# Optimization experiments

Measured on AMD Instinct MI355X. Metric: run time of the kernel, lower is better.

## Reference

```python
import jax, jax.numpy as jnp
import numpy as np

B, T, C, H = 4, 2048, 768, 64

def setup_inputs() -> dict:
    key = jax.random.key(0)
    k1, k2, k3, k4 = jax.random.split(key, 4)
    x = jax.random.normal(k1, (B, T, C), dtype=jnp.float32)
    # Dense kernels (glorot-ish scale)
    s = 1.0 / np.sqrt(C)
    Wq = jax.random.normal(k2, (C, H), dtype=jnp.float32) * s
    Wk = jax.random.normal(k3, (C, H), dtype=jnp.float32) * s
    Wv = jax.random.normal(k4, (C, H), dtype=jnp.float32) * s
    return {"x": x, "Wq": Wq, "Wk": Wk, "Wv": Wv}

def reference(x, Wq, Wk, Wv):
    # q, k, v: [B, T, H]
    q = jnp.einsum('btc,ch->bth', x, Wq)
    k = jnp.einsum('btc,ch->bth', x, Wk)
    v = jnp.einsum('btc,ch->bth', x, Wv)
    scale = k.shape[-1] ** -0.5
    # scores: [B, T, T]
    scores = jnp.einsum('bth,bsh->bts', q, k) * scale
    # causal mask: lower-triangular allowed
    causal = jnp.tril(jnp.ones((T, T), dtype=bool))
    scores = jnp.where(causal, scores, -jnp.inf)
    weights = jax.nn.softmax(scores, axis=-1)
    # dropout is inactive at inference (Keras default training=False)
    out = jnp.einsum('bts,bsh->bth', weights, v)
    return out
```

## Files before the change

### kernel.cpp

```cpp
#include <hip/hip_runtime.h>
#include <hip/hip_bf16.h>
#include <math.h>

constexpr int BB = 4;
constexpr int TT = 2048;
constexpr int CC = 768;
constexpr int HH = 64;
constexpr int NSPLIT = 8;

#define QSCALE 0.1803368801111204f

typedef __attribute__((ext_vector_type(8))) short bf16x8;
typedef __attribute__((ext_vector_type(4))) float f32x4;

__device__ inline ushort f2bf(float f) {
    uint u = __float_as_uint(f);
    u += 0x7fffu + ((u >> 16) & 1u);
    return (ushort)(u >> 16);
}

__device__ inline float fexp2(float x) { return __builtin_amdgcn_exp2f(x); }

__device__ inline bf16x8 cvt8(const float4 a, const float4 b) {
    union { bf16x8 v; __hip_bfloat162 h[4]; } u;
    u.h[0] = __float22bfloat162_rn(make_float2(a.x, a.y));
    u.h[1] = __float22bfloat162_rn(make_float2(a.z, a.w));
    u.h[2] = __float22bfloat162_rn(make_float2(b.x, b.y));
    u.h[3] = __float22bfloat162_rn(make_float2(b.z, b.w));
    return u.v;
}

__global__ __launch_bounds__(256) void prep_w(const float* __restrict__ Wq,
                                              const float* __restrict__ Wk,
                                              const float* __restrict__ Wv,
                                              ushort* __restrict__ Wt) {
    const int k0  = blockIdx.x * 64;
    const int mat = blockIdx.y;
    const float* W = (mat == 0) ? Wq : (mat == 1) ? Wk : Wv;
    __shared__ ushort tile[64 * 66];
    const int tid = threadIdx.x;

    for (int i = tid; i < 1024; i += 256) {
        int kk = i >> 4, c = i & 15;
        float4 f = ((const float4*)W)[(k0 + kk) * 16 + c];
        ushort* d = &tile[kk * 66 + c * 4];
        d[0] = f2bf(f.x); d[1] = f2bf(f.y); d[2] = f2bf(f.z); d[3] = f2bf(f.w);
    }
    __syncthreads();
    for (int i = tid; i < 512; i += 256) {
        int n = i >> 3, c8 = i & 7;
        bf16x8 v;
        #pragma unroll
        for (int j = 0; j < 8; ++j)
            ((ushort*)&v)[j] = tile[(c8 * 8 + j) * 66 + n];
        *(bf16x8*)&Wt[(size_t)(mat * 64 + n) * CC + k0 + c8 * 8] = v;
    }
}

__global__ __launch_bounds__(256) void qkv_mfma(const float* __restrict__ x,
                                                const ushort* __restrict__ Wt,
                                                ushort* __restrict__ qg,
                                                ushort* __restrict__ kg,
                                                ushort* __restrict__ vtg) {
    __shared__ ushort vts[64 * 24];
    const int tid  = threadIdx.x;
    const int row0 = blockIdx.x * 16;
    const int lane = tid & 63, w = tid >> 6;
    const int l15  = lane & 15, quad = lane >> 4;
    const int cg   = w * 48;

    f32x4 acc[3];
    #pragma unroll
    for (int i = 0; i < 3; ++i) acc[i] = (f32x4){0.f, 0.f, 0.f, 0.f};

    const float*  xrow  = x + (size_t)(row0 + l15) * CC;
    const ushort* wbase = Wt + (size_t)(cg + l15) * CC + quad * 8;

    float4 xb[4][2];
    bf16x8 wb[4][3];
    #pragma unroll
    for (int i = 0; i < 4; ++i) {
        const float4* xp = (const float4*)(xrow + i * 32) + quad * 2;
        xb[i][0] = xp[0];
        xb[i][1] = xp[1];
        #pragma unroll
        for (int nt = 0; nt < 3; ++nt)
            wb[i][nt] = *(const bf16x8*)(wbase + (size_t)nt * 16 * CC + i * 32);
    }

    #pragma unroll
    for (int kc = 0; kc < 24; ++kc) {
        const int cur = kc & 3;
        bf16x8 a  = cvt8(xb[cur][0], xb[cur][1]);
        bf16x8 w0 = wb[cur][0], w1 = wb[cur][1], w2 = wb[cur][2];
        const int nx = kc + 4;
        if (nx < 24) {
            const float4* xp = (const float4*)(xrow + nx * 32) + quad * 2;
            xb[cur][0] = xp[0];
            xb[cur][1] = xp[1];
            #pragma unroll
            for (int nt = 0; nt < 3; ++nt)
                wb[cur][nt] = *(const bf16x8*)(wbase + (size_t)nt * 16 * CC + nx * 32);
        }
        acc[0] = __builtin_amdgcn_mfma_f32_16x16x32_bf16(a, w0, acc[0], 0, 0, 0);
        acc[1] = __builtin_amdgcn_mfma_f32_16x16x32_bf16(a, w1, acc[1], 0, 0, 0);
        acc[2] = __builtin_amdgcn_mfma_f32_16x16x32_bf16(a, w2, acc[2], 0, 0, 0);
    }

    #pragma unroll
    for (int nt = 0; nt < 3; ++nt) {
        int n = cg + nt * 16 + l15;
        #pragma unroll
        for (int r = 0; r < 4; ++r) {
            int row = row0 + quad * 4 + r;
            float vacc = acc[nt][r];
            if (n < 64)       qg[(size_t)row * HH + n] = f2bf(vacc * QSCALE);
            else if (n < 128) kg[(size_t)row * HH + (n - 64)] = f2bf(vacc);
            else              vts[(n - 128) * 24 + (quad * 4 + r)] = f2bf(vacc);
        }
    }
    __syncthreads();
    if (tid < 128) {
        int h = tid >> 1, p = tid & 1;
        int b = row0 >> 11, tl = row0 & 2047;
        bf16x8 v = *(const bf16x8*)&vts[h * 24 + p * 8];
        *(bf16x8*)&vtg[(size_t)b * (HH * TT) + (size_t)h * TT + tl + p * 8] = v;
    }
}

__global__ __launch_bounds__(128) void attn_split(const ushort* __restrict__ qg,
                                                  const ushort* __restrict__ kg,
                                                  const ushort* __restrict__ vtg,
                                                  float* __restrict__ Op,
                                                  float* __restrict__ ml) {
    const int qt2 = blockIdx.x, b = blockIdx.y, split = blockIdx.z;
    const int tid  = threadIdx.x;
    const int lane = tid & 63, w = tid >> 6;
    const int l15  = lane & 15, quad = lane >> 4;
    const int t0   = qt2 * 32;
    const int pidx = ((b * 64 + qt2) << 3) + split;

    const int ntile = (qt2 >> 1) + 1;
    const int lo = (ntile * split) >> 3;
    const int hi = (ntile * (split + 1)) >> 3;

    if (lo >= hi) {
        float4 z = (float4){0.f, 0.f, 0.f, 0.f};
        float4* op4 = (float4*)(Op + (size_t)pidx * 2048);
        #pragma unroll
        for (int j = 0; j < 4; ++j) op4[tid * 4 + j] = z;
        if (tid < 32) {
            ml[pidx * 64 + tid]      = -1e30f;
            ml[pidx * 64 + 32 + tid] = 0.f;
        }
        return;
    }

    __shared__ ushort Ps[2][16 * 72];

    const ushort* qp = &qg[(size_t)(b * TT + t0 + w * 16 + l15) * HH + quad * 8];
    bf16x8 qa0 = *(const bf16x8*)qp;
    bf16x8 qa1 = *(const bf16x8*)(qp + 32);

    const ushort* kbb = &kg[(size_t)(b * TT + l15) * HH + quad * 8];
    const ushort* vbb = &vtg[(size_t)b * (HH * TT) + (size_t)l15 * TT + quad * 8];

    f32x4 po[4];
    #pragma unroll
    for (int i = 0; i < 4; ++i) po[i] = (f32x4){0.f, 0.f, 0.f, 0.f};
    float mrun[4] = {-1e30f, -1e30f, -1e30f, -1e30f};
    float lrun[4] = {0.f, 0.f, 0.f, 0.f};

    bf16x8 kb[8], vb[8];
    #pragma unroll
    for (int nt = 0; nt < 4; ++nt) {
        const ushort* kp = kbb + (size_t)(lo * 64 + nt * 16) * HH;
        kb[2 * nt]     = *(const bf16x8*)kp;
        kb[2 * nt + 1] = *(const bf16x8*)(kp + 32);
    }

    for (int st = lo; st < hi; ++st) {
        f32x4 sf[4];
        #pragma unroll
        for (int nt = 0; nt < 4; ++nt) {
            f32x4 z = (f32x4){0.f, 0.f, 0.f, 0.f};
            z = __builtin_amdgcn_mfma_f32_16x16x32_bf16(qa0, kb[2 * nt], z, 0, 0, 0);
            sf[nt] = __builtin_amdgcn_mfma_f32_16x16x32_bf16(qa1, kb[2 * nt + 1], z, 0, 0, 0);
        }
        if (st + 1 < hi) {
            #pragma unroll
            for (int nt = 0; nt < 4; ++nt) {
                const ushort* kp = kbb + (size_t)((st + 1) * 64 + nt * 16) * HH;
                kb[2 * nt]     = *(const bf16x8*)kp;
                kb[2 * nt + 1] = *(const bf16x8*)(kp + 32);
            }
        }
        #pragma unroll
        for (int jj = 0; jj < 4; ++jj) {
            const ushort* vp = vbb + (size_t)(jj * 16) * TT + st * 64;
            vb[2 * jj]     = *(const bf16x8*)vp;
            vb[2 * jj + 1] = *(const bf16x8*)(vp + 32);
        }

        float p[4][4];
        float rm[4] = {-1e30f, -1e30f, -1e30f, -1e30f};
        if (st == ntile - 1) {
            #pragma unroll
            for (int nt = 0; nt < 4; ++nt) {
                int s_abs = st * 64 + nt * 16 + l15;
                #pragma unroll
                for (int r = 0; r < 4; ++r) {
                    int t_abs = t0 + w * 16 + quad * 4 + r;
                    float v = (s_abs > t_abs) ? -1e30f : sf[nt][r];
                    p[nt][r] = v;
                    rm[r] = fmaxf(rm[r], v);
                }
            }
        } else {
            #pragma unroll
            for (int nt = 0; nt < 4; ++nt)
                #pragma unroll
                for (int r = 0; r < 4; ++r) {
                    p[nt][r] = sf[nt][r];
                    rm[r] = fmaxf(rm[r], sf[nt][r]);
                }
        }
        float alpha[4], rs[4] = {0.f, 0.f, 0.f, 0.f};
        #pragma unroll
        for (int r = 0; r < 4; ++r) {
            float v = rm[r];
            v = fmaxf(v, __shfl_xor(v, 1, 64));
            v = fmaxf(v, __shfl_xor(v, 2, 64));
            v = fmaxf(v, __shfl_xor(v, 4, 64));
            v = fmaxf(v, __shfl_xor(v, 8, 64));
            float mnew = fmaxf(mrun[r], v);
            alpha[r] = fexp2(mrun[r] - mnew);
            mrun[r] = mnew;
        }
        #pragma unroll
        for (int nt = 0; nt < 4; ++nt)
            #pragma unroll
            for (int r = 0; r < 4; ++r) {
                float e = fexp2(p[nt][r] - mrun[r]);
                p[nt][r] = e;
                rs[r] += e;
            }
        #pragma unroll
        for (int r = 0; r < 4; ++r) {
            float v = rs[r];
            v += __shfl_xor(v, 1, 64);
            v += __shfl_xor(v, 2, 64);
            v += __shfl_xor(v, 4, 64);
            v += __shfl_xor(v, 8, 64);
            lrun[r] = lrun[r] * alpha[r] + v;
        }
        #pragma unroll
        for (int jj = 0; jj < 4; ++jj)
            #pragma unroll
            for (int r = 0; r < 4; ++r)
                po[jj][r] *= alpha[r];

        #pragma unroll
        for (int nt = 0; nt < 4; ++nt)
            #pragma unroll
            for (int r = 0; r < 4; ++r)
                Ps[w][(quad * 4 + r) * 72 + nt * 16 + l15] = f2bf(p[nt][r]);
        bf16x8 pa0 = *(const bf16x8*)&Ps[w][l15 * 72 + quad * 8];
        bf16x8 pa1 = *(const bf16x8*)&Ps[w][l15 * 72 + 32 + quad * 8];

        #pragma unroll
        for (int jj = 0; jj < 4; ++jj) {
            po[jj] = __builtin_amdgcn_mfma_f32_16x16x32_bf16(pa0, vb[2 * jj], po[jj], 0, 0, 0);
            po[jj] = __builtin_amdgcn_mfma_f32_16x16x32_bf16(pa1, vb[2 * jj + 1], po[jj], 0, 0, 0);
        }
    }

    #pragma unroll
    for (int jj = 0; jj < 4; ++jj)
        #pragma unroll
        for (int r = 0; r < 4; ++r)
            Op[(size_t)pidx * 2048 + (w * 16 + quad * 4 + r) * 64 + jj * 16 + l15] =
                po[jj][r];
    if (l15 == 0) {
        #pragma unroll
        for (int r = 0; r < 4; ++r) {
            int row = w * 16 + quad * 4 + r;
            ml[pidx * 64 + row]      = mrun[r];
            ml[pidx * 64 + 32 + row] = lrun[r];
        }
    }
}

__global__ __launch_bounds__(256) void attn_merge(const float* __restrict__ Op,
                                                  const float* __restrict__ ml,
                                                  float* __restrict__ out) {
    const int tid = threadIdx.x;
    const int w = tid >> 6, lane = tid & 63;
    const int row = blockIdx.x * 4 + w;
    const int b = row >> 11, t = row & 2047;
    const int qt2 = t >> 5, rl = t & 31;
    const int pbase = ((b * 64 + qt2) << 3);

    float m[NSPLIT], l[NSPLIT];
    #pragma unroll
    for (int i = 0; i < NSPLIT; ++i) {
        m[i] = ml[(pbase + i) * 64 + rl];
        l[i] = ml[(pbase + i) * 64 + 32 + rl];
    }
    float M = -1e30f;
    #pragma unroll
    for (int i = 0; i < NSPLIT; ++i) M = fmaxf(M, m[i]);
    float wgt[NSPLIT], L = 0.f;
    #pragma unroll
    for (int i = 0; i < NSPLIT; ++i) {
        wgt[i] = fexp2(m[i] - M);
        L += wgt[i] * l[i];
    }
    float acc = 0.f;
    #pragma unroll
    for (int i = 0; i < NSPLIT; ++i)
        acc += wgt[i] * Op[(size_t)(pbase + i) * 2048 + rl * 64 + lane];
    out[(size_t)row * HH + lane] = acc / L;
}

extern "C" void kernel_launch(void* const* d_in, const int* in_sizes, int n_in,
                              void* d_out, int out_size, void* d_ws, size_t ws_size,
                              hipStream_t stream)
{
    const float* x  = (const float*)d_in[0];
    const float* Wq = (const float*)d_in[1];
    const float* Wk = (const float*)d_in[2];
    const float* Wv = (const float*)d_in[3];
    float* out = (float*)d_out;

    ushort* qg  = (ushort*)d_ws;
    ushort* kg  = qg  + (size_t)BB * TT * HH;
    ushort* vtg = kg  + (size_t)BB * TT * HH;
    ushort* Wt  = vtg + (size_t)BB * TT * HH;
    float*  Op  = (float*)(Wt + (size_t)3 * HH * CC);
    float*  ml  = Op + (size_t)2048 * 2048;

    prep_w    <<<dim3(12, 3),           dim3(256), 0, stream>>>(Wq, Wk, Wv, Wt);
    qkv_mfma  <<<dim3((BB * TT) / 16),  dim3(256), 0, stream>>>(x, Wt, qg, kg, vtg);
    attn_split<<<dim3(64, BB, NSPLIT),  dim3(128), 0, stream>>>(qg, kg, vtg, Op, ml);
    attn_merge<<<dim3((BB * TT) / 4),   dim3(256), 0, stream>>>(Op, ml, out);
}
```

Baseline: 135.2 us.

## Fuse split-KV merge into attention kernel via last-block atomic counter

Removes the separate attn_merge launch. Each split block publishes its partial output and m/l statistics, fences, and increments a per-group atomic counter. The last-arriving block of each query group merges all eight partials and writes the final output. This saves a kernel launch and lets the merge read partials that are likely still in cache, at the cost of an added memset, atomics, fences and a serial merge done by a single 128-thread block per group.

```diff
diff --git a/kernel.cpp b/kernel.cpp
--- a/kernel.cpp
+++ b/kernel.cpp
@@ -128,21 +128,27 @@
     }
 }
 
-__global__ __launch_bounds__(128) void attn_split(const ushort* __restrict__ qg,
+__global__ __launch_bounds__(128) void attn_fused(const ushort* __restrict__ qg,
                                                   const ushort* __restrict__ kg,
                                                   const ushort* __restrict__ vtg,
                                                   float* __restrict__ Op,
-                                                  float* __restrict__ ml) {
+                                                  float* __restrict__ ml,
+                                                  int* __restrict__ cnt,
+                                                  float* __restrict__ out) {
     const int qt2 = blockIdx.x, b = blockIdx.y, split = blockIdx.z;
     const int tid  = threadIdx.x;
     const int lane = tid & 63, w = tid >> 6;
     const int l15  = lane & 15, quad = lane >> 4;
     const int t0   = qt2 * 32;
-    const int pidx = ((b * 64 + qt2) << 3) + split;
+    const int grp  = b * 64 + qt2;
+    const int pidx = (grp << 3) + split;
 
     const int ntile = (qt2 >> 1) + 1;
     const int lo = (ntile * split) >> 3;
     const int hi = (ntile * (split + 1)) >> 3;
+
+    __shared__ ushort Ps[2][16 * 72];
+    __shared__ int sOld;
 
     if (lo >= hi) {
         float4 z = (float4){0.f, 0.f, 0.f, 0.f};
@@ -153,174 +159,169 @@
             ml[pidx * 64 + tid]      = -1e30f;
             ml[pidx * 64 + 32 + tid] = 0.f;
         }
-        return;
-    }
-
-    __shared__ ushort Ps[2][16 * 72];
-
-    const ushort* qp = &qg[(size_t)(b * TT + t0 + w * 16 + l15) * HH + quad * 8];
-    bf16x8 qa0 = *(const bf16x8*)qp;
-    bf16x8 qa1 = *(const bf16x8*)(qp + 32);
-
-    const ushort* kbb = &kg[(size_t)(b * TT + l15) * HH + quad * 8];
-    const ushort* vbb = &vtg[(size_t)b * (HH * TT) + (size_t)l15 * TT + quad * 8];
-
-    f32x4 po[4];
-    #pragma unroll
-    for (int i = 0; i < 4; ++i) po[i] = (f32x4){0.f, 0.f, 0.f, 0.f};
-    float mrun[4] = {-1e30f, -1e30f, -1e30f, -1e30f};
-    float lrun[4] = {0.f, 0.f, 0.f, 0.f};
-
-    bf16x8 kb[8], vb[8];
-    #pragma unroll
-    for (int nt = 0; nt < 4; ++nt) {
-        const ushort* kp = kbb + (size_t)(lo * 64 + nt * 16) * HH;
-        kb[2 * nt]     = *(const bf16x8*)kp;
-        kb[2 * nt + 1] = *(const bf16x8*)(kp + 32);
-    }
-
-    for (int st = lo; st < hi; ++st) {
-        f32x4 sf[4];
+    } else {
+        const ushort* qp = &qg[(size_t)(b * TT + t0 + w * 16 + l15) * HH + quad * 8];
+        bf16x8 qa0 = *(const bf16x8*)qp;
+        bf16x8 qa1 = *(const bf16x8*)(qp + 32);
+
+        const ushort* kbb = &kg[(size_t)(b * TT + l15) * HH + quad * 8];
+        const ushort* vbb = &vtg[(size_t)b * (HH * TT) + (size_t)l15 * TT + quad * 8];
+
+        f32x4 po[4];
+        #pragma unroll
+        for (int i = 0; i < 4; ++i) po[i] = (f32x4){0.f, 0.f, 0.f, 0.f};
+        float mrun[4] = {-1e30f, -1e30f, -1e30f, -1e30f};
+        float lrun[4] = {0.f, 0.f, 0.f, 0.f};
+
+        bf16x8 kb[8], vb[8];
         #pragma unroll
         for (int nt = 0; nt < 4; ++nt) {
-            f32x4 z = (f32x4){0.f, 0.f, 0.f, 0.f};
-            z = __builtin_amdgcn_mfma_f32_16x16x32_bf16(qa0, kb[2 * nt], z, 0, 0, 0);
-            sf[nt] = __builtin_amdgcn_mfma_f32_16x16x32_bf16(qa1, kb[2 * nt + 1], z, 0, 0, 0);
-        }
-        if (st + 1 < hi) {
+            const ushort* kp = kbb + (size_t)(lo * 64 + nt * 16) * HH;
+            kb[2 * nt]     = *(const bf16x8*)kp;
+            kb[2 * nt + 1] = *(const bf16x8*)(kp + 32);
+        }
+
+        for (int st = lo; st < hi; ++st) {
+            f32x4 sf[4];
             #pragma unroll
             for (int nt = 0; nt < 4; ++nt) {
-                const ushort* kp = kbb + (size_t)((st + 1) * 64 + nt * 16) * HH;
-                kb[2 * nt]     = *(const bf16x8*)kp;
-                kb[2 * nt + 1] = *(const bf16x8*)(kp + 32);
-            }
-        }
-        #pragma unroll
-        for (int jj = 0; jj < 4; ++jj) {
-            const ushort* vp = vbb + (size_t)(jj * 16) * TT + st * 64;
-            vb[2 * jj]     = *(const bf16x8*)vp;
-            vb[2 * jj + 1] = *(const bf16x8*)(vp + 32);
-        }
-
-        float p[4][4];
-        float rm[4] = {-1e30f, -1e30f, -1e30f, -1e30f};
-        if (st == ntile - 1) {
-            #pragma unroll
-            for (int nt = 0; nt < 4; ++nt) {
-                int s_abs = st * 64 + nt * 16 + l15;
+                f32x4 z = (f32x4){0.f, 0.f, 0.f, 0.f};
+                z = __builtin_amdgcn_mfma_f32_16x16x32_bf16(qa0, kb[2 * nt], z, 0, 0, 0);
+                sf[nt] = __builtin_amdgcn_mfma_f32_16x16x32_bf16(qa1, kb[2 * nt + 1], z, 0, 0, 0);
+            }
+            if (st + 1 < hi) {
+                #pragma unroll
+                for (int nt = 0; nt < 4; ++nt) {
+                    const ushort* kp = kbb + (size_t)((st + 1) * 64 + nt * 16) * HH;
+                    kb[2 * nt]     = *(const bf16x8*)kp;
+                    kb[2 * nt + 1] = *(const bf16x8*)(kp + 32);
+                }
+            }
+            #pragma unroll
+            for (int jj = 0; jj < 4; ++jj) {
+                const ushort* vp = vbb + (size_t)(jj * 16) * TT + st * 64;
+                vb[2 * jj]     = *(const bf16x8*)vp;
+                vb[2 * jj + 1] = *(const bf16x8*)(vp + 32);
+            }
+
+            float p[4][4];
+            float rm[4] = {-1e30f, -1e30f, -1e30f, -1e30f};
+            if (st == ntile - 1) {
+                #pragma unroll
+                for (int nt = 0; nt < 4; ++nt) {
+                    int s_abs = st * 64 + nt * 16 + l15;
+                    #pragma unroll
+                    for (int r = 0; r < 4; ++r) {
+                        int t_abs = t0 + w * 16 + quad * 4 + r;
+                        float v = (s_abs > t_abs) ? -1e30f : sf[nt][r];
+                        p[nt][r] = v;
+                        rm[r] = fmaxf(rm[r], v);
+                    }
+                }
+            } else {
+                #pragma unroll
+                for (int nt = 0; nt < 4; ++nt)
+                    #pragma unroll
+                    for (int r = 0; r < 4; ++r) {
+                        p[nt][r] = sf[nt][r];
+                        rm[r] = fmaxf(rm[r], sf[nt][r]);
+                    }
+            }
+            float alpha[4], rs[4] = {0.f, 0.f, 0.f, 0.f};
+            #pragma unroll
+            for (int r = 0; r < 4; ++r) {
+                float v = rm[r];
+                v = fmaxf(v, __shfl_xor(v, 1, 64));
+                v = fmaxf(v, __shfl_xor(v, 2, 64));
+                v = fmaxf(v, __shfl_xor(v, 4, 64));
+                v = fmaxf(v, __shfl_xor(v, 8, 64));
+                float mnew = fmaxf(mrun[r], v);
+                alpha[r] = fexp2(mrun[r] - mnew);
+                mrun[r] = mnew;
+            }
+            #pragma unroll
+            for (int nt = 0; nt < 4; ++nt)
                 #pragma unroll
                 for (int r = 0; r < 4; ++r) {
-                    int t_abs = t0 + w * 16 + quad * 4 + r;
-                    float v = (s_abs > t_abs) ? -1e30f : sf[nt][r];
-                    p[nt][r] = v;
-                    rm[r] = fmaxf(rm[r], v);
+                    float e = fexp2(p[nt][r] - mrun[r]);
+                    p[nt][r] = e;
+                    rs[r] += e;
                 }
-            }
-        } else {
+            #pragma unroll
+            for (int r = 0; r < 4; ++r) {
+                float v = rs[r];
+                v += __shfl_xor(v, 1, 64);
+                v += __shfl_xor(v, 2, 64);
+                v += __shfl_xor(v, 4, 64);
+                v += __shfl_xor(v, 8, 64);
+                lrun[r] = lrun[r] * alpha[r] + v;
+            }
+            #pragma unroll
+            for (int jj = 0; jj < 4; ++jj)
+                #pragma unroll
+                for (int r = 0; r < 4; ++r)
+                    po[jj][r] *= alpha[r];
+
             #pragma unroll
             for (int nt = 0; nt < 4; ++nt)
                 #pragma unroll
-                for (int r = 0; r < 4; ++r) {
-                    p[nt][r] = sf[nt][r];
-                    rm[r] = fmaxf(rm[r], sf[nt][r]);
-                }
-        }
-        float alpha[4], rs[4] = {0.f, 0.f, 0.f, 0.f};
-        #pragma unroll
-        for (int r = 0; r < 4; ++r) {
-            float v = rm[r];
-            v = fmaxf(v, __shfl_xor(v, 1, 64));
-            v = fmaxf(v, __shfl_xor(v, 2, 64));
-            v = fmaxf(v, __shfl_xor(v, 4, 64));
-            v = fmaxf(v, __shfl_xor(v, 8, 64));
-            float mnew = fmaxf(mrun[r], v);
-            alpha[r] = fexp2(mrun[r] - mnew);
-            mrun[r] = mnew;
-        }
-        #pragma unroll
-        for (int nt = 0; nt < 4; ++nt)
+                for (int r = 0; r < 4; ++r)
+                    Ps[w][(quad * 4 + r) * 72 + nt * 16 + l15] = f2bf(p[nt][r]);
+            bf16x8 pa0 = *(const bf16x8*)&Ps[w][l15 * 72 + quad * 8];
+            bf16x8 pa1 = *(const bf16x8*)&Ps[w][l15 * 72 + 32 + quad * 8];
+
+            #pragma unroll
+            for (int jj = 0; jj < 4; ++jj) {
+                po[jj] = __builtin_amdgcn_mfma_f32_16x16x32_bf16(pa0, vb[2 * jj], po[jj], 0, 0, 0);
+                po[jj] = __builtin_amdgcn_mfma_f32_16x16x32_bf16(pa1, vb[2 * jj + 1], po[jj], 0, 0, 0);
+            }
+        }
+
+        #pragma unroll
+        for (int jj = 0; jj < 4; ++jj)
+            #pragma unroll
+            for (int r = 0; r < 4; ++r)
+                Op[(size_t)pidx * 2048 + (w * 16 + quad * 4 + r) * 64 + jj * 16 + l15] =
+                    po[jj][r];
+        if (l15 == 0) {
             #pragma unroll
             for (int r = 0; r < 4; ++r) {
-                float e = fexp2(p[nt][r] - mrun[r]);
-                p[nt][r] = e;
-                rs[r] += e;
-            }
-        #pragma unroll
-        for (int r = 0; r < 4; ++r) {
-            float v = rs[r];
-            v += __shfl_xor(v, 1, 64);
-            v += __shfl_xor(v, 2, 64);
-            v += __shfl_xor(v, 4, 64);
-            v += __shfl_xor(v, 8, 64);
-            lrun[r] = lrun[r] * alpha[r] + v;
-        }
-        #pragma unroll
-        for (int jj = 0; jj < 4; ++jj)
-            #pragma unroll
-            for (int r = 0; r < 4; ++r)
-                po[jj][r] *= alpha[r];
-
-        #pragma unroll
-        for (int nt = 0; nt < 4; ++nt)
-            #pragma unroll
-            for (int r = 0; r < 4; ++r)
-                Ps[w][(quad * 4 + r) * 72 + nt * 16 + l15] = f2bf(p[nt][r]);
-        bf16x8 pa0 = *(const bf16x8*)&Ps[w][l15 * 72 + quad * 8];
-        bf16x8 pa1 = *(const bf16x8*)&Ps[w][l15 * 72 + 32 + quad * 8];
-
-        #pragma unroll
-        for (int jj = 0; jj < 4; ++jj) {
-            po[jj] = __builtin_amdgcn_mfma_f32_16x16x32_bf16(pa0, vb[2 * jj], po[jj], 0, 0, 0);
-            po[jj] = __builtin_amdgcn_mfma_f32_16x16x32_bf16(pa1, vb[2 * jj + 1], po[jj], 0, 0, 0);
-        }
-    }
-
-    #pragma unroll
-    for (int jj = 0; jj < 4; ++jj)
-        #pragma unroll
-        for (int r = 0; r < 4; ++r)
-            Op[(size_t)pidx * 2048 + (w * 16 + quad * 4 + r) * 64 + jj * 16 + l15] =
-                po[jj][r];
-    if (l15 == 0) {
-        #pragma unroll
-        for (int r = 0; r < 4; ++r) {
-            int row = w * 16 + quad * 4 + r;
-            ml[pidx * 64 + row]      = mrun[r];
-            ml[pidx * 64 + 32 + row] = lrun[r];
-        }
-    }
-}
-
-__global__ __launch_bounds__(256) void attn_merge(const float* __restrict__ Op,
-                                                  const float* __restrict__ ml,
-                                                  float* __restrict__ out) {
-    const int tid = threadIdx.x;
-    const int w = tid >> 6, lane = tid & 63;
-    const int row = blockIdx.x * 4 + w;
-    const int b = row >> 11, t = row & 2047;
-    const int qt2 = t >> 5, rl = t & 31;
-    const int pbase = ((b * 64 + qt2) << 3);
-
-    float m[NSPLIT], l[NSPLIT];
-    #pragma unroll
-    for (int i = 0; i < NSPLIT; ++i) {
-        m[i] = ml[(pbase + i) * 64 + rl];
-        l[i] = ml[(pbase + i) * 64 + 32 + rl];
-    }
-    float M = -1e30f;
-    #pragma unroll
-    for (int i = 0; i < NSPLIT; ++i) M = fmaxf(M, m[i]);
-    float wgt[NSPLIT], L = 0.f;
-    #pragma unroll
-    for (int i = 0; i < NSPLIT; ++i) {
-        wgt[i] = fexp2(m[i] - M);
-        L += wgt[i] * l[i];
-    }
-    float acc = 0.f;
-    #pragma unroll
-    for (int i = 0; i < NSPLIT; ++i)
-        acc += wgt[i] * Op[(size_t)(pbase + i) * 2048 + rl * 64 + lane];
-    out[(size_t)row * HH + lane] = acc / L;
+                int row = w * 16 + quad * 4 + r;
+                ml[pidx * 64 + row]      = mrun[r];
+                ml[pidx * 64 + 32 + row] = lrun[r];
+            }
+        }
+    }
+
+    __threadfence();
+    if (tid == 0) sOld = atomicAdd(&cnt[grp], 1);
+    __syncthreads();
+    if (sOld != NSPLIT - 1) return;
+    __threadfence();
+
+    const int pbase = grp << 3;
+    for (int rr = w; rr < 32; rr += 2) {
+        float m[NSPLIT], l[NSPLIT];
+        #pragma unroll
+        for (int i = 0; i < NSPLIT; ++i) {
+            m[i] = ml[(pbase + i) * 64 + rr];
+            l[i] = ml[(pbase + i) * 64 + 32 + rr];
+        }
+        float M = -1e30f;
+        #pragma unroll
+        for (int i = 0; i < NSPLIT; ++i) M = fmaxf(M, m[i]);
+        float wgt[NSPLIT], L = 0.f;
+        #pragma unroll
+        for (int i = 0; i < NSPLIT; ++i) {
+            wgt[i] = fexp2(m[i] - M);
+            L += wgt[i] * l[i];
+        }
+        float acc = 0.f;
+        #pragma unroll
+        for (int i = 0; i < NSPLIT; ++i)
+            acc += wgt[i] * Op[(size_t)(pbase + i) * 2048 + rr * 64 + lane];
+        out[(size_t)(b * TT + t0 + rr) * HH + lane] = acc / L;
+    }
 }
 
 extern "C" void kernel_launch(void* const* d_in, const int* in_sizes, int n_in,
@@ -339,9 +340,10 @@
     ushort* Wt  = vtg + (size_t)BB * TT * HH;
     float*  Op  = (float*)(Wt + (size_t)3 * HH * CC);
     float*  ml  = Op + (size_t)2048 * 2048;
-
+    int*    cnt = (int*)(ml + (size_t)2048 * 64);
+
+    hipMemsetAsync(cnt, 0, 256 * sizeof(int), stream);
     prep_w    <<<dim3(12, 3),           dim3(256), 0, stream>>>(Wq, Wk, Wv, Wt);
     qkv_mfma  <<<dim3((BB * TT) / 16),  dim3(256), 0, stream>>>(x, Wt, qg, kg, vtg);
-    attn_split<<<dim3(64, BB, NSPLIT),  dim3(128), 0, stream>>>(qg, kg, vtg, Op, ml);
-    attn_merge<<<dim3((BB * TT) / 4),   dim3(256), 0, stream>>>(Op, ml, out);
-}
+    attn_fused<<<dim3(64, BB, NSPLIT),  dim3(128), 0, stream>>>(qg, kg, vtg, Op, ml, cnt, out);
+}
```

Measured after the change: 268.8 us. 98.9% more time.

## Stage QKV projection tiles in double-buffered LDS with 32-row blocks

Applied to the files above, without the earlier changes.

The QKV projection kernel now handles 32 rows per block instead of 16. The x and weight tiles are staged through double-buffered shared memory, 64 columns of K at a time. Each wave computes a 16x96 output tile with six accumulators, which raises operand reuse and halves the number of blocks and redundant weight reads from global memory. In exchange it adds LDS traffic, a barrier per K step, and higher LDS use per block (about 60KB), which may limit occupancy.

```diff
diff --git a/kernel.cpp b/kernel.cpp
--- a/kernel.cpp
+++ b/kernel.cpp
@@ -62,68 +62,93 @@
                                                 ushort* __restrict__ qg,
                                                 ushort* __restrict__ kg,
                                                 ushort* __restrict__ vtg) {
-    __shared__ ushort vts[64 * 24];
+    __shared__ ushort xs[2][32 * 72];
+    __shared__ ushort ws[2][192 * 72];
+    __shared__ ushort vts[64 * 40];
     const int tid  = threadIdx.x;
-    const int row0 = blockIdx.x * 16;
+    const int row0 = blockIdx.x * 32;
     const int lane = tid & 63, w = tid >> 6;
     const int l15  = lane & 15, quad = lane >> 4;
-    const int cg   = w * 48;
-
-    f32x4 acc[3];
-    #pragma unroll
-    for (int i = 0; i < 3; ++i) acc[i] = (f32x4){0.f, 0.f, 0.f, 0.f};
-
-    const float*  xrow  = x + (size_t)(row0 + l15) * CC;
-    const ushort* wbase = Wt + (size_t)(cg + l15) * CC + quad * 8;
-
-    float4 xb[4][2];
-    bf16x8 wb[4][3];
-    #pragma unroll
-    for (int i = 0; i < 4; ++i) {
-        const float4* xp = (const float4*)(xrow + i * 32) + quad * 2;
-        xb[i][0] = xp[0];
-        xb[i][1] = xp[1];
-        #pragma unroll
-        for (int nt = 0; nt < 3; ++nt)
-            wb[i][nt] = *(const bf16x8*)(wbase + (size_t)nt * 16 * CC + i * 32);
-    }
-
-    #pragma unroll
-    for (int kc = 0; kc < 24; ++kc) {
-        const int cur = kc & 3;
-        bf16x8 a  = cvt8(xb[cur][0], xb[cur][1]);
-        bf16x8 w0 = wb[cur][0], w1 = wb[cur][1], w2 = wb[cur][2];
-        const int nx = kc + 4;
-        if (nx < 24) {
-            const float4* xp = (const float4*)(xrow + nx * 32) + quad * 2;
-            xb[cur][0] = xp[0];
-            xb[cur][1] = xp[1];
-            #pragma unroll
-            for (int nt = 0; nt < 3; ++nt)
-                wb[cur][nt] = *(const bf16x8*)(wbase + (size_t)nt * 16 * CC + nx * 32);
-        }
-        acc[0] = __builtin_amdgcn_mfma_f32_16x16x32_bf16(a, w0, acc[0], 0, 0, 0);
-        acc[1] = __builtin_amdgcn_mfma_f32_16x16x32_bf16(a, w1, acc[1], 0, 0, 0);
-        acc[2] = __builtin_amdgcn_mfma_f32_16x16x32_bf16(a, w2, acc[2], 0, 0, 0);
-    }
-
-    #pragma unroll
-    for (int nt = 0; nt < 3; ++nt) {
+    const int m0   = (w & 1) * 16;
+    const int cg   = (w >> 1) * 96;
+
+    f32x4 acc[6];
+    #pragma unroll
+    for (int i = 0; i < 6; ++i) acc[i] = (f32x4){0.f, 0.f, 0.f, 0.f};
+
+    const int ar = tid >> 3, ac = tid & 7;
+    const float* xg = x + (size_t)(row0 + ar) * CC + ac * 8;
+
+    {
+        const float4* xp = (const float4*)xg;
+        *(bf16x8*)&xs[0][ar * 72 + ac * 8] = cvt8(xp[0], xp[1]);
+        #pragma unroll
+        for (int j = 0; j < 6; ++j) {
+            int c = tid + j * 256;
+            int rw = c >> 3, cc = c & 7;
+            *(bf16x8*)&ws[0][rw * 72 + cc * 8] =
+                *(const bf16x8*)&Wt[(size_t)rw * CC + cc * 8];
+        }
+    }
+    __syncthreads();
+
+    for (int kc = 0; kc < 12; ++kc) {
+        const int cur = kc & 1, nxt = cur ^ 1;
+        const bool have = (kc + 1 < 12);
+
+        float4 f0, f1;
+        bf16x8 wreg[6];
+        if (have) {
+            const float4* xp = (const float4*)(xg + (kc + 1) * 64);
+            f0 = xp[0]; f1 = xp[1];
+            #pragma unroll
+            for (int j = 0; j < 6; ++j) {
+                int c = tid + j * 256;
+                int rw = c >> 3, cc = c & 7;
+                wreg[j] = *(const bf16x8*)&Wt[(size_t)rw * CC + (kc + 1) * 64 + cc * 8];
+            }
+        }
+
+        #pragma unroll
+        for (int ks = 0; ks < 2; ++ks) {
+            bf16x8 a = *(const bf16x8*)&xs[cur][(m0 + l15) * 72 + ks * 32 + quad * 8];
+            #pragma unroll
+            for (int nt = 0; nt < 6; ++nt) {
+                bf16x8 bfr = *(const bf16x8*)
+                    &ws[cur][(cg + nt * 16 + l15) * 72 + ks * 32 + quad * 8];
+                acc[nt] = __builtin_amdgcn_mfma_f32_16x16x32_bf16(a, bfr, acc[nt], 0, 0, 0);
+            }
+        }
+
+        if (have) {
+            *(bf16x8*)&xs[nxt][ar * 72 + ac * 8] = cvt8(f0, f1);
+            #pragma unroll
+            for (int j = 0; j < 6; ++j) {
+                int c = tid + j * 256;
+                int rw = c >> 3, cc = c & 7;
+                *(bf16x8*)&ws[nxt][rw * 72 + cc * 8] = wreg[j];
+            }
+        }
+        __syncthreads();
+    }
+
+    #pragma unroll
+    for (int nt = 0; nt < 6; ++nt) {
         int n = cg + nt * 16 + l15;
         #pragma unroll
         for (int r = 0; r < 4; ++r) {
-            int row = row0 + quad * 4 + r;
+            int row = row0 + m0 + quad * 4 + r;
             float vacc = acc[nt][r];
             if (n < 64)       qg[(size_t)row * HH + n] = f2bf(vacc * QSCALE);
             else if (n < 128) kg[(size_t)row * HH + (n - 64)] = f2bf(vacc);
-            else              vts[(n - 128) * 24 + (quad * 4 + r)] = f2bf(vacc);
+            else              vts[(n - 128) * 40 + (m0 + quad * 4 + r)] = f2bf(vacc);
         }
     }
     __syncthreads();
-    if (tid < 128) {
-        int h = tid >> 1, p = tid & 1;
+    {
+        int h = tid >> 2, p = tid & 3;
         int b = row0 >> 11, tl = row0 & 2047;
-        bf16x8 v = *(const bf16x8*)&vts[h * 24 + p * 8];
+        bf16x8 v = *(const bf16x8*)&vts[h * 40 + p * 8];
         *(bf16x8*)&vtg[(size_t)b * (HH * TT) + (size_t)h * TT + tl + p * 8] = v;
     }
 }
@@ -341,7 +366,7 @@
     float*  ml  = Op + (size_t)2048 * 2048;
 
     prep_w    <<<dim3(12, 3),           dim3(256), 0, stream>>>(Wq, Wk, Wv, Wt);
-    qkv_mfma  <<<dim3((BB * TT) / 16),  dim3(256), 0, stream>>>(x, Wt, qg, kg, vtg);
+    qkv_mfma  <<<dim3((BB * TT) / 32),  dim3(256), 0, stream>>>(x, Wt, qg, kg, vtg);
     attn_split<<<dim3(64, BB, NSPLIT),  dim3(128), 0, stream>>>(qg, kg, vtg, Op, ml);
     attn_merge<<<dim3((BB * TT) / 4),   dim3(256), 0, stream>>>(Op, ml, out);
 }
```

Result: faster. 118.8 us (-12.1%).
